# Kernel tuning notes

Measured on AMD Instinct MI355X. Metric: run time of the kernel, lower is better.

Reference implementation:

```python
import jax, jax.numpy as jnp
import numpy as np

B, N, D, H = 128, 32, 256, 1024

def setup_inputs() -> dict:
    key = jax.random.key(0)
    k1, k2, k3, k4, k5 = jax.random.split(key, 5)
    attribute_embeddings = jax.random.normal(k1, (B, N, D), dtype=jnp.float32)
    # MLP params: Linear(D->H), ReLU, Linear(H->D). Kaiming-uniform-ish init scale.
    W1 = jax.random.normal(k2, (D, H), dtype=jnp.float32) * (1.0 / np.sqrt(D))
    b1 = jax.random.normal(k3, (H,), dtype=jnp.float32) * 0.01
    W2 = jax.random.normal(k4, (H, D), dtype=jnp.float32) * (1.0 / np.sqrt(H))
    b2 = jax.random.normal(k5, (D,), dtype=jnp.float32) * 0.01
    return {"attribute_embeddings": attribute_embeddings, "W1": W1, "b1": b1, "W2": W2, "b2": b2}

def reference(attribute_embeddings, W1, b1, W2, b2):
    x = attribute_embeddings  # [B, N, D]
    # All pairwise elementwise products: [B, N, N, D]
    pair = x[:, :, None, :] * x[:, None, :, :]
    # Batched 2-layer MLP over the last dim
    h = jax.nn.relu(jnp.einsum('bijd,dh->bijh', pair, W1) + b1)  # [B, N, N, H]
    out = jnp.einsum('bijh,hd->bijd', h, W2) + b2                # [B, N, N, D]
    # Original sums over dim=1 (the i index) -> [B, N, D]
    return jnp.sum(out, axis=1)
```

## Files before the change

kernel.cpp:

```cpp
#include <hip/hip_runtime.h>

typedef __attribute__((ext_vector_type(8))) _Float16 f16x8;
typedef __attribute__((ext_vector_type(4))) _Float16 f16x4;
typedef __attribute__((ext_vector_type(4))) float f32x4;

typedef __attribute__((address_space(3))) unsigned int lds_u32;
typedef const __attribute__((address_space(1))) unsigned int g_u32;

#define DEV_INLINE __device__ __forceinline__

constexpr int B_ = 128, N_ = 32, D_ = 256, H_ = 1024;
constexpr int XPAD = 260;

constexpr int LDS_MAIN = 69632;

DEV_INLINE void gload_lds16(const void* g, void* l) {
    __builtin_amdgcn_global_load_lds((g_u32*)g, (lds_u32*)l, 16, 0, 0);
}

#define BARRIER() asm volatile("s_barrier" ::: "memory")

__global__ void prep2(const float* __restrict__ W1, const float* __restrict__ W2,
                      _Float16* __restrict__ W1T, _Float16* __restrict__ W2T) {
    __shared__ float tile[32][36];
    const int t = threadIdx.x;
    const int r = t >> 3, cq = (t & 7) * 4;
    int bb = blockIdx.x;
    if (bb < 256) {
        int tk = bb >> 5, th = bb & 31;
        *(f32x4*)&tile[r][cq] = *(const f32x4*)(W1 + (size_t)(tk * 32 + r) * 1024 + th * 32 + cq);
        __syncthreads();
        f16x4 o;
        #pragma unroll
        for (int q = 0; q < 4; ++q) o[q] = (_Float16)tile[cq + q][r];
        *(f16x4*)(W1T + (size_t)(th * 32 + r) * 256 + tk * 32 + cq) = o;
    } else {
        bb -= 256;
        int th = bb >> 3, td = bb & 7;
        *(f32x4*)&tile[r][cq] = *(const f32x4*)(W2 + (size_t)(th * 32 + r) * 256 + td * 32 + cq);
        __syncthreads();
        f16x4 o;
        #pragma unroll
        for (int q = 0; q < 4; ++q) o[q] = (_Float16)tile[cq + q][r];
        *(f16x4*)(W2T + (size_t)(td * 32 + r) * 1024 + th * 32 + cq) = o;
    }
}

__global__ __launch_bounds__(512, 4)
void interaction_main(const float* __restrict__ Xg, const float* __restrict__ b1g,
                      const _Float16* __restrict__ W1T, _Float16* __restrict__ sg) {
    __shared__ __align__(16) unsigned char smem[LDS_MAIN];

    const int tid = threadIdx.x;
    const int w = tid >> 6, l = tid & 63, l15 = l & 15, lg = l >> 4;
    const int bid = blockIdx.x;
    const int b = bid >> 2, jg = bid & 3;
    const int j0 = jg * 8;

    float* Xs  = (float*)smem;
    float* b1s = (float*)(smem + 65536);

    {
        const float* xb = Xg + (size_t)b * (N_ * D_);
        int row = tid >> 4, c0 = (tid & 15) * 16;
        #pragma unroll
        for (int q = 0; q < 4; ++q)
            *(f32x4*)(Xs + row * XPAD + c0 + q * 4) = *(const f32x4*)(xb + row * 256 + c0 + q * 4);
        b1s[tid]       = b1g[tid];
        b1s[tid + 512] = b1g[tid + 512];
    }
    __syncthreads();

    f16x8 afrag[2][8];
    {
        const float* xj = Xs + (j0 + w) * XPAD;
        #pragma unroll
        for (int ks = 0; ks < 8; ++ks) {
            int k0 = ks * 32 + lg * 8;
            f32x4 xjA = *(const f32x4*)(xj + k0);
            f32x4 xjB = *(const f32x4*)(xj + k0 + 4);
            #pragma unroll
            for (int rt = 0; rt < 2; ++rt) {
                const float* xi = Xs + (rt * 16 + l15) * XPAD + k0;
                f32x4 a0 = *(const f32x4*)(xi);
                f32x4 a1 = *(const f32x4*)(xi + 4);
                f16x8 a;
                a[0] = (_Float16)(a0[0] * xjA[0]);
                a[1] = (_Float16)(a0[1] * xjA[1]);
                a[2] = (_Float16)(a0[2] * xjA[2]);
                a[3] = (_Float16)(a0[3] * xjA[3]);
                a[4] = (_Float16)(a1[0] * xjB[0]);
                a[5] = (_Float16)(a1[1] * xjB[1]);
                a[6] = (_Float16)(a1[2] * xjB[2]);
                a[7] = (_Float16)(a1[3] * xjB[3]);
                afrag[rt][ks] = a;
            }
        }
    }
    __syncthreads();

    auto stage = [&](int c) {
        const int bufbase = (c & 1) * 32768;
        #pragma unroll
        for (int p = 0; p < 4; ++p) {
            int hc   = ((p * 8 + w) << 1) + (l >> 5);
            int srco = ((l & 31) ^ (hc & 7)) << 3;
            const _Float16* src = W1T + (size_t)(c * 64 + hc) * 256 + srco;
            void* dst = smem + bufbase + (p * 8 + w) * 1024;
            gload_lds16(src, dst);
        }
    };

    stage(0);
    const size_t srow = (size_t)(b * 32 + j0 + w) * 1024;

    for (int c = 0; c < 16; ++c) {
        if (c < 15) {
            stage(c + 1);
            asm volatile("s_waitcnt vmcnt(4)" ::: "memory");
        } else {
            asm volatile("s_waitcnt vmcnt(0)" ::: "memory");
        }
        BARRIER();

        const int bufbase = (c & 1) * 32768;
        f32x4 acc0[4] = {};
        f32x4 acc1[4] = {};
        __builtin_amdgcn_s_setprio(1);
        #pragma unroll
        for (int ks = 0; ks < 8; ++ks) {
            #pragma unroll
            for (int ct = 0; ct < 4; ++ct) {
                int hc = ct * 16 + l15;
                int boff = bufbase + hc * 512 + ((ks * 64 + lg * 16) ^ ((hc & 7) << 4));
                f16x8 bfr = *(const f16x8*)(smem + boff);
                acc0[ct] = __builtin_amdgcn_mfma_f32_16x16x32_f16(afrag[0][ks], bfr, acc0[ct], 0, 0, 0);
                acc1[ct] = __builtin_amdgcn_mfma_f32_16x16x32_f16(afrag[1][ks], bfr, acc1[ct], 0, 0, 0);
            }
        }
        __builtin_amdgcn_s_setprio(0);

        #pragma unroll
        for (int ct = 0; ct < 4; ++ct) {
            int hcol = c * 64 + ct * 16 + l15;
            float bv = b1s[hcol];
            float v = 0.f;
            #pragma unroll
            for (int r = 0; r < 4; ++r)
                v += fmaxf(acc0[ct][r] + bv, 0.f) + fmaxf(acc1[ct][r] + bv, 0.f);
            v += __shfl_xor(v, 16, 64);
            v += __shfl_xor(v, 32, 64);
            if (l < 16) sg[srow + hcol] = (_Float16)v;
        }
        BARRIER();
    }
}

__global__ __launch_bounds__(256, 4)
void layer2_kernel(const _Float16* __restrict__ sg, const _Float16* __restrict__ W2T,
                   const float* __restrict__ b2g, float* __restrict__ outg) {
    const int tid = threadIdx.x;
    const int w = tid >> 6, l = tid & 63, l15 = l & 15, lg = l >> 4;
    const int m0 = blockIdx.x * 16;

    f32x4 acc[4] = {};
    const _Float16* arow = sg  + (size_t)(m0 + l15) * 1024 + lg * 8;
    const _Float16* brow = W2T + (size_t)(w * 64 + l15) * 1024 + lg * 8;
    #pragma unroll
    for (int ks = 0; ks < 32; ++ks) {
        f16x8 af = *(const f16x8*)(arow + ks * 32);
        #pragma unroll
        for (int ct = 0; ct < 4; ++ct) {
            f16x8 bf = *(const f16x8*)(brow + (size_t)ct * 16 * 1024 + ks * 32);
            acc[ct] = __builtin_amdgcn_mfma_f32_16x16x32_f16(af, bf, acc[ct], 0, 0, 0);
        }
    }
    #pragma unroll
    for (int ct = 0; ct < 4; ++ct) {
        int d = w * 64 + ct * 16 + l15;
        float bb = 32.f * b2g[d];
        #pragma unroll
        for (int r = 0; r < 4; ++r)
            outg[(size_t)(m0 + lg * 4 + r) * 256 + d] = acc[ct][r] + bb;
    }
}

extern "C" void kernel_launch(void* const* d_in, const int* in_sizes, int n_in,
                              void* d_out, int out_size, void* d_ws, size_t ws_size,
                              hipStream_t stream) {
    const float* X  = (const float*)d_in[0];
    const float* W1 = (const float*)d_in[1];
    const float* b1 = (const float*)d_in[2];
    const float* W2 = (const float*)d_in[3];
    const float* b2 = (const float*)d_in[4];
    float* out = (float*)d_out;

    _Float16* W1T = (_Float16*)d_ws;
    _Float16* W2T = W1T + 262144;
    _Float16* sgl = W2T + 262144;

    prep2<<<dim3(512), dim3(256), 0, stream>>>(W1, W2, W1T, W2T);
    interaction_main<<<dim3(512), dim3(512), 0, stream>>>(X, b1, W1T, sgl);
    layer2_kernel<<<dim3(256), dim3(256), 0, stream>>>(sgl, W2T, b2, out);
}
```

Baseline: 157.5 us.

## Fuse layer-2 GEMM into interaction kernel and double j-rows per block

Each block now handles 16 j indices instead of 8, so every W1T chunk staged into LDS feeds twice as many MFMAs. The per-j hidden sums stay in LDS as fp16 and a fused second GEMM against W2T computes the output directly, dropping the separate layer2 kernel and the global round trip of the intermediate. In exchange, LDS use grows to about 100KB, occupancy drops to 2 blocks per CU, the grid halves to 256 blocks, and register pressure rises from the doubled A fragments and accumulators.

Result: faster. 136.3 us (-13.5%).

```diff
diff --git a/kernel.cpp b/kernel.cpp
--- a/kernel.cpp
+++ b/kernel.cpp
@@ -11,8 +11,9 @@
 
 constexpr int B_ = 128, N_ = 32, D_ = 256, H_ = 1024;
 constexpr int XPAD = 260;
-
-constexpr int LDS_MAIN = 69632;
+constexpr int SROW = 1032;
+
+constexpr int LDS_MAIN = 102656;
 
 DEV_INLINE void gload_lds16(const void* g, void* l) {
     __builtin_amdgcn_global_load_lds((g_u32*)g, (lds_u32*)l, 16, 0, 0);
@@ -46,19 +47,21 @@
     }
 }
 
-__global__ __launch_bounds__(512, 4)
+__global__ __launch_bounds__(512, 2)
 void interaction_main(const float* __restrict__ Xg, const float* __restrict__ b1g,
-                      const _Float16* __restrict__ W1T, _Float16* __restrict__ sg) {
+                      const float* __restrict__ b2g, const _Float16* __restrict__ W1T,
+                      const _Float16* __restrict__ W2T, float* __restrict__ outg) {
     __shared__ __align__(16) unsigned char smem[LDS_MAIN];
 
     const int tid = threadIdx.x;
     const int w = tid >> 6, l = tid & 63, l15 = l & 15, lg = l >> 4;
     const int bid = blockIdx.x;
-    const int b = bid >> 2, jg = bid & 3;
-    const int j0 = jg * 8;
-
-    float* Xs  = (float*)smem;
-    float* b1s = (float*)(smem + 65536);
+    const int b = bid >> 1, jg = bid & 1;
+    const int j0 = jg * 16;
+
+    float*     Xs  = (float*)smem;
+    _Float16*  s16 = (_Float16*)(smem + 65536);
+    float*     b1s = (float*)(smem + 98560);
 
     {
         const float* xb = Xg + (size_t)b * (N_ * D_);
@@ -71,29 +74,33 @@
     }
     __syncthreads();
 
-    f16x8 afrag[2][8];
+    f16x8 afrag[2][2][8];
     {
-        const float* xj = Xs + (j0 + w) * XPAD;
+        const float* xja = Xs + (j0 + w) * XPAD;
+        const float* xjb = Xs + (j0 + 8 + w) * XPAD;
         #pragma unroll
         for (int ks = 0; ks < 8; ++ks) {
             int k0 = ks * 32 + lg * 8;
-            f32x4 xjA = *(const f32x4*)(xj + k0);
-            f32x4 xjB = *(const f32x4*)(xj + k0 + 4);
+            f32x4 jA0 = *(const f32x4*)(xja + k0);
+            f32x4 jA1 = *(const f32x4*)(xja + k0 + 4);
+            f32x4 jB0 = *(const f32x4*)(xjb + k0);
+            f32x4 jB1 = *(const f32x4*)(xjb + k0 + 4);
             #pragma unroll
             for (int rt = 0; rt < 2; ++rt) {
                 const float* xi = Xs + (rt * 16 + l15) * XPAD + k0;
-                f32x4 a0 = *(const f32x4*)(xi);
-                f32x4 a1 = *(const f32x4*)(xi + 4);
-                f16x8 a;
-                a[0] = (_Float16)(a0[0] * xjA[0]);
-                a[1] = (_Float16)(a0[1] * xjA[1]);
-                a[2] = (_Float16)(a0[2] * xjA[2]);
-                a[3] = (_Float16)(a0[3] * xjA[3]);
-                a[4] = (_Float16)(a1[0] * xjB[0]);
-                a[5] = (_Float16)(a1[1] * xjB[1]);
-                a[6] = (_Float16)(a1[2] * xjB[2]);
-                a[7] = (_Float16)(a1[3] * xjB[3]);
-                afrag[rt][ks] = a;
+                f32x4 x0 = *(const f32x4*)(xi);
+                f32x4 x1 = *(const f32x4*)(xi + 4);
+                f16x8 a, c;
+                a[0] = (_Float16)(x0[0] * jA0[0]); c[0] = (_Float16)(x0[0] * jB0[0]);
+                a[1] = (_Float16)(x0[1] * jA0[1]); c[1] = (_Float16)(x0[1] * jB0[1]);
+                a[2] = (_Float16)(x0[2] * jA0[2]); c[2] = (_Float16)(x0[2] * jB0[2]);
+                a[3] = (_Float16)(x0[3] * jA0[3]); c[3] = (_Float16)(x0[3] * jB0[3]);
+                a[4] = (_Float16)(x1[0] * jA1[0]); c[4] = (_Float16)(x1[0] * jB1[0]);
+                a[5] = (_Float16)(x1[1] * jA1[1]); c[5] = (_Float16)(x1[1] * jB1[1]);
+                a[6] = (_Float16)(x1[2] * jA1[2]); c[6] = (_Float16)(x1[2] * jB1[2]);
+                a[7] = (_Float16)(x1[3] * jA1[3]); c[7] = (_Float16)(x1[3] * jB1[3]);
+                afrag[0][rt][ks] = a;
+                afrag[1][rt][ks] = c;
             }
         }
     }
@@ -112,7 +119,6 @@
     };
 
     stage(0);
-    const size_t srow = (size_t)(b * 32 + j0 + w) * 1024;
 
     for (int c = 0; c < 16; ++c) {
         if (c < 15) {
@@ -124,8 +130,7 @@
         BARRIER();
 
         const int bufbase = (c & 1) * 32768;
-        f32x4 acc0[4] = {};
-        f32x4 acc1[4] = {};
+        f32x4 acc[2][2][4] = {};
         __builtin_amdgcn_s_setprio(1);
         #pragma unroll
         for (int ks = 0; ks < 8; ++ks) {
@@ -134,8 +139,10 @@
                 int hc = ct * 16 + l15;
                 int boff = bufbase + hc * 512 + ((ks * 64 + lg * 16) ^ ((hc & 7) << 4));
                 f16x8 bfr = *(const f16x8*)(smem + boff);
-                acc0[ct] = __builtin_amdgcn_mfma_f32_16x16x32_f16(afrag[0][ks], bfr, acc0[ct], 0, 0, 0);
-                acc1[ct] = __builtin_amdgcn_mfma_f32_16x16x32_f16(afrag[1][ks], bfr, acc1[ct], 0, 0, 0);
+                acc[0][0][ct] = __builtin_amdgcn_mfma_f32_16x16x32_f16(afrag[0][0][ks], bfr, acc[0][0][ct], 0, 0, 0);
+                acc[0][1][ct] = __builtin_amdgcn_mfma_f32_16x16x32_f16(afrag[0][1][ks], bfr, acc[0][1][ct], 0, 0, 0);
+                acc[1][0][ct] = __builtin_amdgcn_mfma_f32_16x16x32_f16(afrag[1][0][ks], bfr, acc[1][0][ct], 0, 0, 0);
+                acc[1][1][ct] = __builtin_amdgcn_mfma_f32_16x16x32_f16(afrag[1][1][ks], bfr, acc[1][1][ct], 0, 0, 0);
             }
         }
         __builtin_amdgcn_s_setprio(0);
@@ -144,44 +151,48 @@
         for (int ct = 0; ct < 4; ++ct) {
             int hcol = c * 64 + ct * 16 + l15;
             float bv = b1s[hcol];
-            float v = 0.f;
+            float v0 = 0.f, v1 = 0.f;
             #pragma unroll
-            for (int r = 0; r < 4; ++r)
-                v += fmaxf(acc0[ct][r] + bv, 0.f) + fmaxf(acc1[ct][r] + bv, 0.f);
-            v += __shfl_xor(v, 16, 64);
-            v += __shfl_xor(v, 32, 64);
-            if (l < 16) sg[srow + hcol] = (_Float16)v;
+            for (int rt = 0; rt < 2; ++rt)
+                #pragma unroll
+                for (int r = 0; r < 4; ++r) {
+                    v0 += fmaxf(acc[0][rt][ct][r] + bv, 0.f);
+                    v1 += fmaxf(acc[1][rt][ct][r] + bv, 0.f);
+                }
+            v0 += __shfl_xor(v0, 16, 64);
+            v0 += __shfl_xor(v0, 32, 64);
+            v1 += __shfl_xor(v1, 16, 64);
+            v1 += __shfl_xor(v1, 32, 64);
+            if (lg < 2) {
+                int row = w + (lg << 3);
+                s16[row * SROW + hcol] = (_Float16)(lg ? v1 : v0);
+            }
         }
         BARRIER();
     }
-}
-
-__global__ __launch_bounds__(256, 4)
-void layer2_kernel(const _Float16* __restrict__ sg, const _Float16* __restrict__ W2T,
-                   const float* __restrict__ b2g, float* __restrict__ outg) {
-    const int tid = threadIdx.x;
-    const int w = tid >> 6, l = tid & 63, l15 = l & 15, lg = l >> 4;
-    const int m0 = blockIdx.x * 16;
-
-    f32x4 acc[4] = {};
-    const _Float16* arow = sg  + (size_t)(m0 + l15) * 1024 + lg * 8;
-    const _Float16* brow = W2T + (size_t)(w * 64 + l15) * 1024 + lg * 8;
+
+    __syncthreads();
+
+    f32x4 acc2[2] = {};
     #pragma unroll
     for (int ks = 0; ks < 32; ++ks) {
-        f16x8 af = *(const f16x8*)(arow + ks * 32);
-        #pragma unroll
-        for (int ct = 0; ct < 4; ++ct) {
-            f16x8 bf = *(const f16x8*)(brow + (size_t)ct * 16 * 1024 + ks * 32);
-            acc[ct] = __builtin_amdgcn_mfma_f32_16x16x32_f16(af, bf, acc[ct], 0, 0, 0);
+        f16x8 af = *(const f16x8*)(s16 + l15 * SROW + ks * 32 + lg * 8);
+        #pragma unroll
+        for (int t2 = 0; t2 < 2; ++t2) {
+            const _Float16* bp = W2T + (size_t)((w * 2 + t2) * 16 + l15) * 1024 + ks * 32 + lg * 8;
+            f16x8 bf = *(const f16x8*)bp;
+            acc2[t2] = __builtin_amdgcn_mfma_f32_16x16x32_f16(af, bf, acc2[t2], 0, 0, 0);
         }
     }
     #pragma unroll
-    for (int ct = 0; ct < 4; ++ct) {
-        int d = w * 64 + ct * 16 + l15;
+    for (int t2 = 0; t2 < 2; ++t2) {
+        int d = (w * 2 + t2) * 16 + l15;
         float bb = 32.f * b2g[d];
         #pragma unroll
-        for (int r = 0; r < 4; ++r)
-            outg[(size_t)(m0 + lg * 4 + r) * 256 + d] = acc[ct][r] + bb;
+        for (int r = 0; r < 4; ++r) {
+            int jloc = lg * 4 + r;
+            outg[(size_t)(b * 32 + j0 + jloc) * 256 + d] = acc2[t2][r] + bb;
+        }
     }
 }
 
@@ -197,9 +208,7 @@
 
     _Float16* W1T = (_Float16*)d_ws;
     _Float16* W2T = W1T + 262144;
-    _Float16* sgl = W2T + 262144;
 
     prep2<<<dim3(512), dim3(256), 0, stream>>>(W1, W2, W1T, W2T);
-    interaction_main<<<dim3(512), dim3(512), 0, stream>>>(X, b1, W1T, sgl);
-    layer2_kernel<<<dim3(256), dim3(256), 0, stream>>>(sgl, W2T, b2, out);
-}
+    interaction_main<<<dim3(B_ * (N_ / 16)), dim3(512), 0, stream>>>(X, b1, b2, W1T, W2T, out);
+}
```
